# Kernel tuning notes

Measured on AMD Instinct MI355X. Metric: run time of the kernel, lower is better.

The kernel has to match this reference:

```python
import jax, jax.numpy as jnp
import numpy as np

NEAR, FAR = 0.05, 6.0
STEPSIZE = 0.5
ALPHA_INIT = 1e-6
XYZ_MIN = np.array([-1.0, -1.0, -1.0], np.float32)
XYZ_MAX = np.array([1.0, 1.0, 1.0], np.float32)
WORLD = (160, 160, 160)
VOXEL_SIZE = 2.0 / 160.0  # ((prod span)/num_voxels)^(1/3)
N_SAMPLES = int(np.linalg.norm(np.array(WORLD) + 1) / STEPSIZE) + 1  # 558
ACT_SHIFT = float(np.log(1.0 / (1.0 - ALPHA_INIT) - 1.0))


def setup_inputs() -> dict:
    key = jax.random.key(0)
    k1, k2, k3, k4, k5, k6, k7 = jax.random.split(key, 7)
    rays_o = (jax.random.uniform(k1, (8192, 3), jnp.float32) - 0.5) * 1.2  # inside bbox
    rd = jax.random.normal(k2, (8192, 3), jnp.float32)
    rays_d = rd / jnp.linalg.norm(rd, axis=-1, keepdims=True)
    jitter = jax.random.uniform(k3, (8192, 1), jnp.float32)
    em_modes = jax.random.randint(k4, (8192,), 0, 2, jnp.int32)
    density = jax.random.normal(k5, (1, 160, 160, 160), jnp.float32) * 0.1
    off_color = jax.random.normal(k6, (3, 160, 160, 160), jnp.float32) * 0.1
    emo_color = jax.random.normal(k7, (3, 160, 160, 160), jnp.float32) * 0.1
    return {"rays_o": rays_o, "rays_d": rays_d, "jitter": jitter, "em_modes": em_modes,
            "density": density, "off_color": off_color, "emo_color": emo_color}


def grid_sampler(pts, grid):
    """Trilinear interp, align_corners=True, zero padding. grid [C,Nx,Ny,Nz], pts [...,3] -> [...,C]."""
    C = grid.shape[0]
    sizes = np.array(grid.shape[1:], np.int32)
    lead = pts.shape[:-1]
    t = (pts.reshape(-1, 3) - XYZ_MIN) / (XYZ_MAX - XYZ_MIN)
    idx = t * (jnp.asarray(sizes, pts.dtype) - 1)  # voxel-space coords
    i0 = jnp.floor(idx).astype(jnp.int32)
    f = idx - i0.astype(pts.dtype)
    out = jnp.zeros((i0.shape[0], C), grid.dtype)
    for corner in range(8):
        off = np.array([(corner >> 2) & 1, (corner >> 1) & 1, corner & 1], np.int32)
        ci = i0 + off  # [N,3]
        w = jnp.prod(jnp.where(off[None, :] == 1, f, 1.0 - f), axis=-1)  # [N]
        valid = jnp.all((ci >= 0) & (ci < sizes[None, :]), axis=-1)
        cc = jnp.clip(ci, 0, sizes[None, :] - 1)
        vals = grid[:, cc[:, 0], cc[:, 1], cc[:, 2]].T  # [N,C]
        out = out + (w * valid)[:, None] * vals
    return out.reshape(*lead, C)


def sample_ray(rays_o, rays_d, jitter):
    vec = jnp.where(rays_d == 0, 1e-6, rays_d)
    rate_a = (XYZ_MAX - rays_o) / vec
    rate_b = (XYZ_MIN - rays_o) / vec
    t_min = jnp.clip(jnp.minimum(rate_a, rate_b).max(-1), NEAR, FAR)
    t_max = jnp.clip(jnp.maximum(rate_a, rate_b).min(-1), NEAR, FAR)
    mask_out = t_max <= t_min  # [R]
    rng = jnp.arange(N_SAMPLES, dtype=rays_o.dtype)[None, :] + jitter  # [R,S]
    step = STEPSIZE * VOXEL_SIZE * rng
    interpx = t_min[:, None] + step / jnp.linalg.norm(rays_d, axis=-1, keepdims=True)
    rays_pts = rays_o[:, None, :] + rays_d[:, None, :] * interpx[..., None]  # [R,S,3]
    mask_out = mask_out[:, None] | ((rays_pts < XYZ_MIN) | (rays_pts > XYZ_MAX)).any(-1)
    return rays_pts, mask_out


def reference(rays_o, rays_d, jitter, em_modes, density, off_color, emo_color):
    rays_pts, mask_out = sample_ray(rays_o, rays_d, jitter)
    dens = grid_sampler(rays_pts, density)[..., 0]  # [R,S]
    alpha_all = 1.0 - jnp.exp(-jax.nn.softplus(dens + ACT_SHIFT) * STEPSIZE)
    alpha = jnp.where(mask_out, 0.0, alpha_all)
    p = jnp.clip(1.0 - alpha, 1e-10, None)
    alphainv_cum = jnp.concatenate([jnp.ones_like(p[..., :1]), jnp.cumprod(p, -1)], -1)  # [R,S+1]
    weights = alpha * alphainv_cum[..., :-1]
    on_mask = (em_modes == 1)[:, None, None]
    emo = jax.nn.sigmoid(grid_sampler(rays_pts, emo_color))
    off = jax.nn.sigmoid(grid_sampler(rays_pts, off_color))
    rgb = jnp.where(on_mask, emo, 0.0) + off  # [R,S,3]
    rgb_marched = (weights[..., None] * rgb).sum(-2)  # [R,3]
    return (alphainv_cum, weights, alphainv_cum[..., -1:], rgb, rgb_marched)
```

## Files before the change

### kernel.cpp

```cpp
#include <hip/hip_runtime.h>
#include <math.h>


namespace {
constexpr int   kR   = 8192;
constexpr int   kS   = 558;
constexpr int   kG   = 160;
constexpr int   kG2  = kG * kG;
constexpr int   kG3  = kG * kG * kG;
constexpr float kNear = 0.05f;
constexpr float kFar  = 6.0f;
constexpr float kStepWorld = 0.5f * (2.0f / 160.0f);
constexpr float kActShift = -13.815509557963774f;
constexpr float kLog2e = 1.4426950408889634f;
}

typedef unsigned int nuint2 __attribute__((ext_vector_type(2)));
typedef unsigned int nuint4 __attribute__((ext_vector_type(4)));
typedef float        nfloat2 __attribute__((ext_vector_type(2)));

__device__ __forceinline__ float fexp(float x) {
  return __builtin_amdgcn_exp2f(x * kLog2e);
}
__device__ __forceinline__ float sigmoidf_(float x) {
  return __builtin_amdgcn_rcpf(1.0f + fexp(-x));
}

__global__ __launch_bounds__(256) void repack_grids(
    const float* __restrict__ density,
    const float* __restrict__ off_c,
    const float* __restrict__ emo_c,
    nuint2* __restrict__ packed)
{
  const int v = blockIdx.x * blockDim.x + threadIdx.x;
  if (v >= kG3) return;
  const float d  = __builtin_nontemporal_load(density + v);
  const float f0 = __builtin_nontemporal_load(off_c + v);
  const float f1 = __builtin_nontemporal_load(off_c + v + kG3);
  const float f2 = __builtin_nontemporal_load(off_c + v + 2 * kG3);
  const float e0 = __builtin_nontemporal_load(emo_c + v);
  const float e1 = __builtin_nontemporal_load(emo_c + v + kG3);
  const float e2 = __builtin_nontemporal_load(emo_c + v + 2 * kG3);
  int qx = __builtin_amdgcn_cvt_pk_fp8_f32(d,  f0, 0,  false);
  qx     = __builtin_amdgcn_cvt_pk_fp8_f32(f1, f2, qx, true);
  int qy = __builtin_amdgcn_cvt_pk_fp8_f32(e0, e1, 0,  false);
  qy     = __builtin_amdgcn_cvt_pk_fp8_f32(e2, 0.0f, qy, true);
  nuint2 q;
  q.x = (unsigned)qx;
  q.y = (unsigned)qy;
  __builtin_nontemporal_store(q, packed + v);
}

__global__ __launch_bounds__(256) void dvgo_fwd(
    const float* __restrict__ rays_o,
    const float* __restrict__ rays_d,
    const float* __restrict__ jitter,
    const int*   __restrict__ em_modes,
    const uint2* __restrict__ packed8,
    float* __restrict__ out)
{
  const int tid  = blockIdx.x * blockDim.x + threadIdx.x;
  const int ray  = tid >> 6;
  const int lane = tid & 63;
  if (ray >= kR) return;

  const float ox = rays_o[ray * 3 + 0];
  const float oy = rays_o[ray * 3 + 1];
  const float oz = rays_o[ray * 3 + 2];
  const float dx = rays_d[ray * 3 + 0];
  const float dy = rays_d[ray * 3 + 1];
  const float dz = rays_d[ray * 3 + 2];
  const float jit = jitter[ray];
  const bool  on  = (em_modes[ray] == 1);

  const float vx = (dx == 0.0f) ? 1e-6f : dx;
  const float vy = (dy == 0.0f) ? 1e-6f : dy;
  const float vz = (dz == 0.0f) ? 1e-6f : dz;
  const float ivx = __builtin_amdgcn_rcpf(vx);
  const float ivy = __builtin_amdgcn_rcpf(vy);
  const float ivz = __builtin_amdgcn_rcpf(vz);
  const float rax = ( 1.0f - ox) * ivx, rbx = (-1.0f - ox) * ivx;
  const float ray_a = ( 1.0f - oy) * ivy, rby = (-1.0f - oy) * ivy;
  const float raz = ( 1.0f - oz) * ivz, rbz = (-1.0f - oz) * ivz;
  float tmin = fmaxf(fmaxf(fminf(rax, rbx), fminf(ray_a, rby)), fminf(raz, rbz));
  float tmax = fminf(fminf(fmaxf(rax, rbx), fmaxf(ray_a, rby)), fmaxf(raz, rbz));
  tmin = fminf(fmaxf(tmin, kNear), kFar);
  tmax = fminf(fmaxf(tmax, kNear), kFar);
  const bool  ray_out = (tmax <= tmin);
  const float stepc = kStepWorld *
      __builtin_amdgcn_rsqf(dx * dx + dy * dy + dz * dz);

  float* out_ainv = out;
  float* out_w    = out + (size_t)kR * (kS + 1);
  float* out_last = out_w + (size_t)kR * kS;
  float* out_rgb  = out_last + kR;
  float* out_rm   = out_rgb + (size_t)kR * kS * 3;

  if (lane == 0)
    __builtin_nontemporal_store(1.0f, out_ainv + (size_t)ray * (kS + 1));

  const float c_base = on ? 1.0f : 0.5f;

  float carry = 1.0f;
  float accr = 0.0f, accg = 0.0f, accb = 0.0f;
  bool dead = false;

  #pragma unroll 1
  for (int chunk = 0; chunk < (kS + 63) / 64; ++chunk) {
    const int  s      = chunk * 64 + lane;
    const bool active = (s < kS);

    if (!dead) {
      const float t  = tmin + stepc * ((float)s + jit);
      const float px = fmaf(dx, t, ox);
      const float py = fmaf(dy, t, oy);
      const float pz = fmaf(dz, t, oz);
      const bool inb = (px >= -1.0f) & (px <= 1.0f) &
                       (py >= -1.0f) & (py <= 1.0f) &
                       (pz >= -1.0f) & (pz <= 1.0f);
      const bool masked = ray_out || !inb;

      const float fx = (px + 1.0f) * 0.5f * (float)(kG - 1);
      const float fy = (py + 1.0f) * 0.5f * (float)(kG - 1);
      const float fz = (pz + 1.0f) * 0.5f * (float)(kG - 1);
      const int ix = (int)floorf(fx);
      const int iy = (int)floorf(fy);
      const int iz = (int)floorf(fz);

      const bool reach = active &&
          (ix >= -1) && (ix <= kG - 1) &&
          (iy >= -1) && (iy <= kG - 1) &&
          (iz >= -1) && (iz <= kG - 1);
      if (__ballot(reach) == 0ull) {
        dead = true;
      } else {
        const float wx = fx - (float)ix;
        const float wy = fy - (float)iy;
        const float wz = fz - (float)iz;
        const float x0 = 1.0f - wx, y0 = 1.0f - wy, z0 = 1.0f - wz;
        const float wxy00 = x0 * y0, wxy01 = x0 * wy;
        const float wxy10 = wx * y0, wxy11 = wx * wy;
        float w8[8];
        w8[0] = wxy00 * z0; w8[1] = wxy00 * wz;
        w8[2] = wxy01 * z0; w8[3] = wxy01 * wz;
        w8[4] = wxy10 * z0; w8[5] = wxy10 * wz;
        w8[6] = wxy11 * z0; w8[7] = wxy11 * wz;

        float dsum = 0.0f;
        float o0 = 0.0f, o1 = 0.0f, o2 = 0.0f;
        float e0 = 0.0f, e1 = 0.0f, e2 = 0.0f;

        const bool interior = active &&
            (ix >= 0) && (ix < kG - 1) &&
            (iy >= 0) && (iy < kG - 1) &&
            (iz >= 0) && (iz < kG - 1);

        if (interior) {
          const int base = (ix * kG + iy) * kG + iz;
          #pragma unroll
          for (int cc = 0; cc < 4; ++cc) {
            const int gi = base + ((cc >> 1) & 1) * kG2 + (cc & 1) * kG;
            const nuint4 q = *(const nuint4*)(packed8 + gi);
            const float w0 = w8[2 * cc + 0];
            const float w1 = w8[2 * cc + 1];
            dsum = fmaf(w0, __builtin_amdgcn_cvt_f32_fp8((int)q.x, 0),
                   fmaf(w1, __builtin_amdgcn_cvt_f32_fp8((int)q.z, 0), dsum));
            o0   = fmaf(w0, __builtin_amdgcn_cvt_f32_fp8((int)q.x, 1),
                   fmaf(w1, __builtin_amdgcn_cvt_f32_fp8((int)q.z, 1), o0));
            o1   = fmaf(w0, __builtin_amdgcn_cvt_f32_fp8((int)q.x, 2),
                   fmaf(w1, __builtin_amdgcn_cvt_f32_fp8((int)q.z, 2), o1));
            o2   = fmaf(w0, __builtin_amdgcn_cvt_f32_fp8((int)q.x, 3),
                   fmaf(w1, __builtin_amdgcn_cvt_f32_fp8((int)q.z, 3), o2));
            if (on) {
              e0 = fmaf(w0, __builtin_amdgcn_cvt_f32_fp8((int)q.y, 0),
                   fmaf(w1, __builtin_amdgcn_cvt_f32_fp8((int)q.w, 0), e0));
              e1 = fmaf(w0, __builtin_amdgcn_cvt_f32_fp8((int)q.y, 1),
                   fmaf(w1, __builtin_amdgcn_cvt_f32_fp8((int)q.w, 1), e1));
              e2 = fmaf(w0, __builtin_amdgcn_cvt_f32_fp8((int)q.y, 2),
                   fmaf(w1, __builtin_amdgcn_cvt_f32_fp8((int)q.w, 2), e2));
            }
          }
        } else if (reach) {
          #pragma unroll
          for (int c = 0; c < 8; ++c) {
            const int cx = ix + ((c >> 2) & 1);
            const int cy = iy + ((c >> 1) & 1);
            const int cz = iz + (c & 1);
            const bool valid = ((unsigned)cx < (unsigned)kG) &
                               ((unsigned)cy < (unsigned)kG) &
                               ((unsigned)cz < (unsigned)kG);
            const float wv = valid ? w8[c] : 0.0f;
            const int gx = min(max(cx, 0), kG - 1);
            const int gy = min(max(cy, 0), kG - 1);
            const int gz = min(max(cz, 0), kG - 1);
            const int gi = (gx * kG + gy) * kG + gz;
            const uint2 q = packed8[gi];
            dsum = fmaf(wv, __builtin_amdgcn_cvt_f32_fp8((int)q.x, 0), dsum);
            o0   = fmaf(wv, __builtin_amdgcn_cvt_f32_fp8((int)q.x, 1), o0);
            o1   = fmaf(wv, __builtin_amdgcn_cvt_f32_fp8((int)q.x, 2), o1);
            o2   = fmaf(wv, __builtin_amdgcn_cvt_f32_fp8((int)q.x, 3), o2);
            if (on) {
              e0 = fmaf(wv, __builtin_amdgcn_cvt_f32_fp8((int)q.y, 0), e0);
              e1 = fmaf(wv, __builtin_amdgcn_cvt_f32_fp8((int)q.y, 1), e1);
              e2 = fmaf(wv, __builtin_amdgcn_cvt_f32_fp8((int)q.y, 2), e2);
            }
          }
        }

        float p = 1.0f;
        if (active && !masked) {
          const float ex = fexp(dsum + kActShift);
          p = fmaxf(__builtin_amdgcn_rsqf(1.0f + ex), 1e-10f);
        }
        const float alpha = 1.0f - p;

        float incl = p;
        #pragma unroll
        for (int o = 1; o < 64; o <<= 1) {
          const float n = __shfl_up(incl, o, 64);
          if (lane >= o) incl *= n;
        }
        float excl = __shfl_up(incl, 1, 64);
        if (lane == 0) excl = 1.0f;
        const float ainv_prev = carry * excl;
        const float ainv_next = carry * incl;
        const float wgt = alpha * ainv_prev;
        carry *= __shfl(incl, 63, 64);

        float rr = sigmoidf_(o0);
        float gg = sigmoidf_(o1);
        float bb = sigmoidf_(o2);
        if (on) {
          rr += sigmoidf_(e0);
          gg += sigmoidf_(e1);
          bb += sigmoidf_(e2);
        }

        if (active) {
          __builtin_nontemporal_store(ainv_next,
              out_ainv + (size_t)ray * (kS + 1) + s + 1);
          __builtin_nontemporal_store(wgt, out_w + (size_t)ray * kS + s);
          const size_t rb = ((size_t)ray * kS + s) * 3;
          nfloat2 rg;
          rg.x = rr; rg.y = gg;
          __builtin_nontemporal_store(rg, (nfloat2*)(out_rgb + rb));
          __builtin_nontemporal_store(bb, out_rgb + rb + 2);
          accr = fmaf(wgt, rr, accr);
          accg = fmaf(wgt, gg, accg);
          accb = fmaf(wgt, bb, accb);
        }
        continue;
      }
    }

    if (active) {
      __builtin_nontemporal_store(carry,
          out_ainv + (size_t)ray * (kS + 1) + s + 1);
      __builtin_nontemporal_store(0.0f, out_w + (size_t)ray * kS + s);
      const size_t rb = ((size_t)ray * kS + s) * 3;
      nfloat2 cb;
      cb.x = c_base; cb.y = c_base;
      __builtin_nontemporal_store(cb, (nfloat2*)(out_rgb + rb));
      __builtin_nontemporal_store(c_base, out_rgb + rb + 2);
    }
  }

  #pragma unroll
  for (int o = 32; o > 0; o >>= 1) {
    accr += __shfl_xor(accr, o, 64);
    accg += __shfl_xor(accg, o, 64);
    accb += __shfl_xor(accb, o, 64);
  }
  if (lane == 0) {
    out_last[ray] = carry;
    out_rm[(size_t)ray * 3 + 0] = accr;
    out_rm[(size_t)ray * 3 + 1] = accg;
    out_rm[(size_t)ray * 3 + 2] = accb;
  }
}

extern "C" void kernel_launch(void* const* d_in, const int* in_sizes, int n_in,
                              void* d_out, int out_size, void* d_ws, size_t ws_size,
                              hipStream_t stream) {
  const float* rays_o  = (const float*)d_in[0];
  const float* rays_d  = (const float*)d_in[1];
  const float* jitter  = (const float*)d_in[2];
  const int*   em      = (const int*)d_in[3];
  const float* density = (const float*)d_in[4];
  const float* off_c   = (const float*)d_in[5];
  const float* emo_c   = (const float*)d_in[6];
  float* out = (float*)d_out;

  nuint2* packed = (nuint2*)d_ws;
  (void)ws_size;

  hipLaunchKernelGGL(repack_grids, dim3((kG3 + 255) / 256), dim3(256), 0,
                     stream, density, off_c, emo_c, packed);

  const int threads = 256;
  const int blocks  = (kR * 64) / threads;
  hipLaunchKernelGGL(dvgo_fwd, dim3(blocks), dim3(threads), 0, stream,
                     rays_o, rays_d, jitter, em, (const uint2*)packed, out);
}
```

Measured before the change: 227.3 us.

## Repack FP8 grids into 2x2x4 bricks with separate density/off and emo planes

The repack kernel now stores the quantized grid in 2x2x4 voxel bricks of 64 bytes, split into two planes: density plus off color in one, emo color in the other. The interior trilinear path fetches eight 4-byte words instead of four 16-byte pairs, and only reads the emo plane for rays with the emission mode on. The aim is better cache-line locality for a trilinear footprint and skipping emo bytes for off rays. In exchange, each sample issues more, smaller loads and needs more index arithmetic.

```diff
diff --git a/kernel.cpp b/kernel.cpp
--- a/kernel.cpp
+++ b/kernel.cpp
@@ -6,18 +6,20 @@
 constexpr int   kR   = 8192;
 constexpr int   kS   = 558;
 constexpr int   kG   = 160;
-constexpr int   kG2  = kG * kG;
 constexpr int   kG3  = kG * kG * kG;
 constexpr float kNear = 0.05f;
 constexpr float kFar  = 6.0f;
 constexpr float kStepWorld = 0.5f * (2.0f / 160.0f);
 constexpr float kActShift = -13.815509557963774f;
 constexpr float kLog2e = 1.4426950408889634f;
-}
-
-typedef unsigned int nuint2 __attribute__((ext_vector_type(2)));
+constexpr int   kBX = 80, kBY = 80, kBZ = 40;
+constexpr int   kNB = kBX * kBY * kBZ;
+constexpr int   kGridWords = kNB * 16;
+}
+
 typedef unsigned int nuint4 __attribute__((ext_vector_type(4)));
 typedef float        nfloat2 __attribute__((ext_vector_type(2)));
+typedef float        nfloat4 __attribute__((ext_vector_type(4)));
 
 __device__ __forceinline__ float fexp(float x) {
   return __builtin_amdgcn_exp2f(x * kLog2e);
@@ -30,25 +32,56 @@
     const float* __restrict__ density,
     const float* __restrict__ off_c,
     const float* __restrict__ emo_c,
-    nuint2* __restrict__ packed)
+    unsigned* __restrict__ gridA,
+    unsigned* __restrict__ gridB)
 {
-  const int v = blockIdx.x * blockDim.x + threadIdx.x;
-  if (v >= kG3) return;
-  const float d  = __builtin_nontemporal_load(density + v);
-  const float f0 = __builtin_nontemporal_load(off_c + v);
-  const float f1 = __builtin_nontemporal_load(off_c + v + kG3);
-  const float f2 = __builtin_nontemporal_load(off_c + v + 2 * kG3);
-  const float e0 = __builtin_nontemporal_load(emo_c + v);
-  const float e1 = __builtin_nontemporal_load(emo_c + v + kG3);
-  const float e2 = __builtin_nontemporal_load(emo_c + v + 2 * kG3);
-  int qx = __builtin_amdgcn_cvt_pk_fp8_f32(d,  f0, 0,  false);
-  qx     = __builtin_amdgcn_cvt_pk_fp8_f32(f1, f2, qx, true);
-  int qy = __builtin_amdgcn_cvt_pk_fp8_f32(e0, e1, 0,  false);
-  qy     = __builtin_amdgcn_cvt_pk_fp8_f32(e2, 0.0f, qy, true);
-  nuint2 q;
-  q.x = (unsigned)qx;
-  q.y = (unsigned)qy;
-  __builtin_nontemporal_store(q, packed + v);
+  const int bid = blockIdx.x * blockDim.x + threadIdx.x;
+  if (bid >= kNB) return;
+  const int bz = bid % kBZ;
+  const int t  = bid / kBZ;
+  const int by = t % kBY;
+  const int bx = t / kBY;
+  const int x0 = bx * 2, y0 = by * 2, z0 = bz * 4;
+
+  unsigned wa[16], wb[16];
+  #pragma unroll
+  for (int lx = 0; lx < 2; ++lx) {
+    #pragma unroll
+    for (int ly = 0; ly < 2; ++ly) {
+      const int vbase = ((x0 + lx) * kG + (y0 + ly)) * kG + z0;
+      const nfloat4 d  = *(const nfloat4*)(density + vbase);
+      const nfloat4 f0 = *(const nfloat4*)(off_c + vbase);
+      const nfloat4 f1 = *(const nfloat4*)(off_c + vbase + kG3);
+      const nfloat4 f2 = *(const nfloat4*)(off_c + vbase + 2 * kG3);
+      const nfloat4 e0 = *(const nfloat4*)(emo_c + vbase);
+      const nfloat4 e1 = *(const nfloat4*)(emo_c + vbase + kG3);
+      const nfloat4 e2 = *(const nfloat4*)(emo_c + vbase + 2 * kG3);
+      #pragma unroll
+      for (int lz = 0; lz < 4; ++lz) {
+        const int s = (lx * 2 + ly) * 4 + lz;
+        int qa = __builtin_amdgcn_cvt_pk_fp8_f32(d[lz],  f0[lz], 0,  false);
+        qa     = __builtin_amdgcn_cvt_pk_fp8_f32(f1[lz], f2[lz], qa, true);
+        int qb = __builtin_amdgcn_cvt_pk_fp8_f32(e0[lz], e1[lz], 0,  false);
+        qb     = __builtin_amdgcn_cvt_pk_fp8_f32(e2[lz], 0.0f,   qb, true);
+        wa[s] = (unsigned)qa;
+        wb[s] = (unsigned)qb;
+      }
+    }
+  }
+  nuint4* oa = (nuint4*)(gridA + (size_t)bid * 16);
+  nuint4* ob = (nuint4*)(gridB + (size_t)bid * 16);
+  #pragma unroll
+  for (int q = 0; q < 4; ++q) {
+    nuint4 va; va.x = wa[4*q]; va.y = wa[4*q+1]; va.z = wa[4*q+2]; va.w = wa[4*q+3];
+    nuint4 vb; vb.x = wb[4*q]; vb.y = wb[4*q+1]; vb.z = wb[4*q+2]; vb.w = wb[4*q+3];
+    __builtin_nontemporal_store(va, oa + q);
+    __builtin_nontemporal_store(vb, ob + q);
+  }
+}
+
+__device__ __forceinline__ int brick_widx(int gx, int gy, int gz) {
+  return (((gx >> 1) * kBY + (gy >> 1)) * kBZ + (gz >> 2)) * 16 +
+         ((gx & 1) * 2 + (gy & 1)) * 4 + (gz & 3);
 }
 
 __global__ __launch_bounds__(256) void dvgo_fwd(
@@ -56,7 +89,8 @@
     const float* __restrict__ rays_d,
     const float* __restrict__ jitter,
     const int*   __restrict__ em_modes,
-    const uint2* __restrict__ packed8,
+    const unsigned* __restrict__ gridA,
+    const unsigned* __restrict__ gridB,
     float* __restrict__ out)
 {
   const int tid  = blockIdx.x * blockDim.x + threadIdx.x;
@@ -156,28 +190,52 @@
             (iz >= 0) && (iz < kG - 1);
 
         if (interior) {
-          const int base = (ix * kG + iy) * kG + iz;
+          const int bx = ix >> 1, lx = ix & 1;
+          const int by = iy >> 1, ly = iy & 1;
+          const int bz = iz >> 2, lz = iz & 3;
+          const int bz1 = (iz + 1) >> 2, lz1 = (iz + 1) & 3;
+          const int r00 = (bx * kBY + by) * kBZ;
+          const int r10 = r00 + lx * (kBY * kBZ);
+          const int r01 = r00 + ly * kBZ;
+          const int r11 = r10 + ly * kBZ;
+          const int sx0 = (lx) * 2,      sx1 = (lx ^ 1) * 2;
+          const int sy0 = ly,            sy1 = ly ^ 1;
+          int widx[8];
+          widx[0] = (r00 + bz ) * 16 + (sx0 + sy0) * 4 + lz;
+          widx[1] = (r00 + bz1) * 16 + (sx0 + sy0) * 4 + lz1;
+          widx[2] = (r01 + bz ) * 16 + (sx0 + sy1) * 4 + lz;
+          widx[3] = (r01 + bz1) * 16 + (sx0 + sy1) * 4 + lz1;
+          widx[4] = (r10 + bz ) * 16 + (sx1 + sy0) * 4 + lz;
+          widx[5] = (r10 + bz1) * 16 + (sx1 + sy0) * 4 + lz1;
+          widx[6] = (r11 + bz ) * 16 + (sx1 + sy1) * 4 + lz;
+          widx[7] = (r11 + bz1) * 16 + (sx1 + sy1) * 4 + lz1;
+
+          unsigned ua[8];
           #pragma unroll
-          for (int cc = 0; cc < 4; ++cc) {
-            const int gi = base + ((cc >> 1) & 1) * kG2 + (cc & 1) * kG;
-            const nuint4 q = *(const nuint4*)(packed8 + gi);
-            const float w0 = w8[2 * cc + 0];
-            const float w1 = w8[2 * cc + 1];
-            dsum = fmaf(w0, __builtin_amdgcn_cvt_f32_fp8((int)q.x, 0),
-                   fmaf(w1, __builtin_amdgcn_cvt_f32_fp8((int)q.z, 0), dsum));
-            o0   = fmaf(w0, __builtin_amdgcn_cvt_f32_fp8((int)q.x, 1),
-                   fmaf(w1, __builtin_amdgcn_cvt_f32_fp8((int)q.z, 1), o0));
-            o1   = fmaf(w0, __builtin_amdgcn_cvt_f32_fp8((int)q.x, 2),
-                   fmaf(w1, __builtin_amdgcn_cvt_f32_fp8((int)q.z, 2), o1));
-            o2   = fmaf(w0, __builtin_amdgcn_cvt_f32_fp8((int)q.x, 3),
-                   fmaf(w1, __builtin_amdgcn_cvt_f32_fp8((int)q.z, 3), o2));
-            if (on) {
-              e0 = fmaf(w0, __builtin_amdgcn_cvt_f32_fp8((int)q.y, 0),
-                   fmaf(w1, __builtin_amdgcn_cvt_f32_fp8((int)q.w, 0), e0));
-              e1 = fmaf(w0, __builtin_amdgcn_cvt_f32_fp8((int)q.y, 1),
-                   fmaf(w1, __builtin_amdgcn_cvt_f32_fp8((int)q.w, 1), e1));
-              e2 = fmaf(w0, __builtin_amdgcn_cvt_f32_fp8((int)q.y, 2),
-                   fmaf(w1, __builtin_amdgcn_cvt_f32_fp8((int)q.w, 2), e2));
+          for (int c = 0; c < 8; ++c) ua[c] = gridA[widx[c]];
+          if (on) {
+            unsigned ub[8];
+            #pragma unroll
+            for (int c = 0; c < 8; ++c) ub[c] = gridB[widx[c]];
+            #pragma unroll
+            for (int c = 0; c < 8; ++c) {
+              const float w = w8[c];
+              dsum = fmaf(w, __builtin_amdgcn_cvt_f32_fp8((int)ua[c], 0), dsum);
+              o0   = fmaf(w, __builtin_amdgcn_cvt_f32_fp8((int)ua[c], 1), o0);
+              o1   = fmaf(w, __builtin_amdgcn_cvt_f32_fp8((int)ua[c], 2), o1);
+              o2   = fmaf(w, __builtin_amdgcn_cvt_f32_fp8((int)ua[c], 3), o2);
+              e0   = fmaf(w, __builtin_amdgcn_cvt_f32_fp8((int)ub[c], 0), e0);
+              e1   = fmaf(w, __builtin_amdgcn_cvt_f32_fp8((int)ub[c], 1), e1);
+              e2   = fmaf(w, __builtin_amdgcn_cvt_f32_fp8((int)ub[c], 2), e2);
+            }
+          } else {
+            #pragma unroll
+            for (int c = 0; c < 8; ++c) {
+              const float w = w8[c];
+              dsum = fmaf(w, __builtin_amdgcn_cvt_f32_fp8((int)ua[c], 0), dsum);
+              o0   = fmaf(w, __builtin_amdgcn_cvt_f32_fp8((int)ua[c], 1), o0);
+              o1   = fmaf(w, __builtin_amdgcn_cvt_f32_fp8((int)ua[c], 2), o1);
+              o2   = fmaf(w, __builtin_amdgcn_cvt_f32_fp8((int)ua[c], 3), o2);
             }
           }
         } else if (reach) {
@@ -193,16 +251,17 @@
             const int gx = min(max(cx, 0), kG - 1);
             const int gy = min(max(cy, 0), kG - 1);
             const int gz = min(max(cz, 0), kG - 1);
-            const int gi = (gx * kG + gy) * kG + gz;
-            const uint2 q = packed8[gi];
-            dsum = fmaf(wv, __builtin_amdgcn_cvt_f32_fp8((int)q.x, 0), dsum);
-            o0   = fmaf(wv, __builtin_amdgcn_cvt_f32_fp8((int)q.x, 1), o0);
-            o1   = fmaf(wv, __builtin_amdgcn_cvt_f32_fp8((int)q.x, 2), o1);
-            o2   = fmaf(wv, __builtin_amdgcn_cvt_f32_fp8((int)q.x, 3), o2);
+            const int wi = brick_widx(gx, gy, gz);
+            const unsigned qa = gridA[wi];
+            dsum = fmaf(wv, __builtin_amdgcn_cvt_f32_fp8((int)qa, 0), dsum);
+            o0   = fmaf(wv, __builtin_amdgcn_cvt_f32_fp8((int)qa, 1), o0);
+            o1   = fmaf(wv, __builtin_amdgcn_cvt_f32_fp8((int)qa, 2), o1);
+            o2   = fmaf(wv, __builtin_amdgcn_cvt_f32_fp8((int)qa, 3), o2);
             if (on) {
-              e0 = fmaf(wv, __builtin_amdgcn_cvt_f32_fp8((int)q.y, 0), e0);
-              e1 = fmaf(wv, __builtin_amdgcn_cvt_f32_fp8((int)q.y, 1), e1);
-              e2 = fmaf(wv, __builtin_amdgcn_cvt_f32_fp8((int)q.y, 2), e2);
+              const unsigned qb = gridB[wi];
+              e0 = fmaf(wv, __builtin_amdgcn_cvt_f32_fp8((int)qb, 0), e0);
+              e1 = fmaf(wv, __builtin_amdgcn_cvt_f32_fp8((int)qb, 1), e1);
+              e2 = fmaf(wv, __builtin_amdgcn_cvt_f32_fp8((int)qb, 2), e2);
             }
           }
         }
@@ -291,14 +350,15 @@
   const float* emo_c   = (const float*)d_in[6];
   float* out = (float*)d_out;
 
-  nuint2* packed = (nuint2*)d_ws;
+  unsigned* gridA = (unsigned*)d_ws;
+  unsigned* gridB = gridA + kGridWords;
   (void)ws_size;
 
-  hipLaunchKernelGGL(repack_grids, dim3((kG3 + 255) / 256), dim3(256), 0,
-                     stream, density, off_c, emo_c, packed);
+  hipLaunchKernelGGL(repack_grids, dim3((kNB + 255) / 256), dim3(256), 0,
+                     stream, density, off_c, emo_c, gridA, gridB);
 
   const int threads = 256;
   const int blocks  = (kR * 64) / threads;
   hipLaunchKernelGGL(dvgo_fwd, dim3(blocks), dim3(threads), 0, stream,
-                     rays_o, rays_d, jitter, em, (const uint2*)packed, out);
-}
+                     rays_o, rays_d, jitter, em, gridA, gridB, out);
+}
```

Measured after the change: 265.6 us. 16.8% more time.
